# Performance work log

Hardware: AMD Instinct MI355X
Metric: run time of the kernel (lower is better)

The kernel has to match this reference:

```python
import jax, jax.numpy as jnp
import numpy as np

THRESH_FACTOR = 0.7


def ternarize(w):
    # w: [in_features, out_features]; per-row (dim 0) delta/alpha stats
    n = w.shape[1]
    abs_w = jnp.abs(w)
    delta = (THRESH_FACTOR / n) * abs_w.sum(axis=1, keepdims=True)  # [in, 1]
    mask = abs_w > delta
    count = mask.sum(axis=1, keepdims=True).astype(w.dtype)
    alpha = jnp.where(mask, abs_w, 0).sum(axis=1, keepdims=True) / count  # [in, 1]
    tern = jnp.where(w > delta, 1.0, jnp.where(w < -delta, -1.0, 0.0)).astype(w.dtype)
    return tern * alpha


def setup_inputs() -> dict:
    key = jax.random.key(0)
    k1, k2, k3 = jax.random.split(key, 3)
    B, IN, OUT = 8192, 4096, 4096
    x = jax.random.normal(k1, (B, IN), dtype=jnp.float32)
    # kaiming-uniform-ish then clamp to [-1, 1] as in the module
    bound_w = float(np.sqrt(6.0 / ((1.0 + 5.0) * IN)))
    weights = jax.random.uniform(k2, (IN, OUT), minval=-bound_w, maxval=bound_w, dtype=jnp.float32)
    weights = jnp.clip(weights, -1.0, 1.0)
    bound_b = 1.0 / float(np.sqrt(IN))
    bias = jax.random.uniform(k3, (OUT,), minval=-bound_b, maxval=bound_b, dtype=jnp.float32)
    return {"x": x, "weights": weights, "bias": bias}


def reference(x, weights, bias):
    w_t = ternarize(weights)
    return jnp.matmul(x, w_t) + bias
```

## Files before the change

### kernel.cpp

```cpp
#include <hip/hip_runtime.h>
#include <stdint.h>
#include <stddef.h>

#define IN_F 4096
#define OUT_F 4096

typedef int i32x4 __attribute__((ext_vector_type(4)));


__device__ static inline void async16(const void* g, void* l) {
    __builtin_amdgcn_global_load_lds(
        (const __attribute__((address_space(1))) unsigned int*)g,
        (__attribute__((address_space(3))) unsigned int*)l,
        16, 0, 0);
}

__device__ static inline double wred_d(double v) {
#pragma unroll
    for (int o = 32; o > 0; o >>= 1) v += __shfl_down(v, o, 64);
    return v;
}

__device__ static inline int wred_i(int v) {
#pragma unroll
    for (int o = 32; o > 0; o >>= 1) v += __shfl_down(v, o, 64);
    return v;
}

__device__ static inline float wred_max(float v) {
#pragma unroll
    for (int o = 32; o > 0; o >>= 1) v = fmaxf(v, __shfl_down(v, o, 64));
    return v;
}


__global__ __launch_bounds__(256) void rowstats_tern_kernel(
    const float* __restrict__ w,
    float* __restrict__ alpha_o,
    unsigned int* __restrict__ Tp) {
    __shared__ double sh_s[4], sh_m[4];
    __shared__ int sh_c[4];
    const int row = blockIdx.x;
    const int t = threadIdx.x;
    const int lane = t & 63, wv = t >> 6;
    const float4* wr = (const float4*)(w + (size_t)row * OUT_F);

    float4 v[4];
    double s = 0.0;
#pragma unroll
    for (int it = 0; it < 4; ++it) {
        v[it] = wr[t + it * 256];
        s += (double)fabsf(v[it].x) + (double)fabsf(v[it].y) +
             (double)fabsf(v[it].z) + (double)fabsf(v[it].w);
    }
    double sw = wred_d(s);
    if (lane == 0) sh_s[wv] = sw;
    __syncthreads();
    const double delta = (sh_s[0] + sh_s[1] + sh_s[2] + sh_s[3]) *
                         (0.7 / (double)OUT_F);

    unsigned int* trow = Tp + (size_t)row * (OUT_F / 4);
    double ms = 0.0;
    int cnt = 0;
#pragma unroll
    for (int it = 0; it < 4; ++it) {
        float f[4] = {v[it].x, v[it].y, v[it].z, v[it].w};
        unsigned int u = 0;
#pragma unroll
        for (int j = 0; j < 4; ++j) {
            double a = (double)fabsf(f[j]);
            if (a > delta) { ms += a; ++cnt; }
            int q = ((double)f[j] > delta) ? 1 :
                    (((double)f[j] < -delta) ? -1 : 0);
            u |= (unsigned int)(q & 0xff) << (j * 8);
        }
        trow[t + it * 256] = u;
    }
    double msw = wred_d(ms);
    int cw = wred_i(cnt);
    if (lane == 0) { sh_m[wv] = msw; sh_c[wv] = cw; }
    __syncthreads();
    if (t == 0) {
        double mtot = sh_m[0] + sh_m[1] + sh_m[2] + sh_m[3];
        int ctot = sh_c[0] + sh_c[1] + sh_c[2] + sh_c[3];
        alpha_o[row] = (float)(mtot / (double)ctot);
    }
}


__global__ __launch_bounds__(256) void transpose_i8_kernel(
    const unsigned int* __restrict__ Tp,
    int8_t* __restrict__ Tt) {
    __shared__ unsigned int ldsb[128 * 33];
    const int t = threadIdx.x;
    const int i0 = blockIdx.y * 128;
    const int j0 = blockIdx.x * 128;

#pragma unroll
    for (int it = 0; it < 4; ++it) {
        int bb = it * 256 + t;
        int rg = bb >> 5;
        int cc = bb & 31;
        unsigned int col[4] = {0u, 0u, 0u, 0u};
#pragma unroll
        for (int k = 0; k < 4; ++k) {
            unsigned int d = Tp[(size_t)(i0 + rg * 4 + k) * (OUT_F / 4) +
                                (j0 >> 2) + cc];
            col[0] |= (d & 0xffu) << (k * 8);
            col[1] |= ((d >> 8) & 0xffu) << (k * 8);
            col[2] |= ((d >> 16) & 0xffu) << (k * 8);
            col[3] |= ((d >> 24) & 0xffu) << (k * 8);
        }
#pragma unroll
        for (int j = 0; j < 4; ++j)
            ldsb[(cc * 4 + j) * 33 + rg] = col[j];
    }
    __syncthreads();
#pragma unroll
    for (int it = 0; it < 4; ++it) {
        int idx = it * 256 + t;
        int rr = idx >> 3;
        int c2 = idx & 7;
        uint4 o;
        o.x = ldsb[rr * 33 + c2 * 4 + 0];
        o.y = ldsb[rr * 33 + c2 * 4 + 1];
        o.z = ldsb[rr * 33 + c2 * 4 + 2];
        o.w = ldsb[rr * 33 + c2 * 4 + 3];
        *(uint4*)(Tt + (size_t)(j0 + rr) * IN_F + i0 + c2 * 16) = o;
    }
}


__global__ __launch_bounds__(256) void xquant_kernel(
    const float* __restrict__ x,
    const float* __restrict__ alpha,
    int8_t* __restrict__ xq,
    float* __restrict__ scale_o) {
    __shared__ float sh_mx[4];
    const int row = blockIdx.x;
    const int t = threadIdx.x;
    const int lane = t & 63, wv = t >> 6;
    const float4* xr = (const float4*)(x + (size_t)row * IN_F);
    const float4* ar = (const float4*)alpha;

    float4 xs[4];
    float mx = 0.0f;
#pragma unroll
    for (int it = 0; it < 4; ++it) {
        float4 v = xr[t + it * 256];
        float4 a = ar[t + it * 256];
        v.x *= a.x; v.y *= a.y; v.z *= a.z; v.w *= a.w;
        xs[it] = v;
        mx = fmaxf(mx, fmaxf(fmaxf(fabsf(v.x), fabsf(v.y)),
                             fmaxf(fabsf(v.z), fabsf(v.w))));
    }
    float mw = wred_max(mx);
    if (lane == 0) sh_mx[wv] = mw;
    __syncthreads();
    const float rmax = fmaxf(fmaxf(sh_mx[0], sh_mx[1]), fmaxf(sh_mx[2], sh_mx[3]));
    const float inv = (rmax > 0.0f) ? (127.0f / rmax) : 0.0f;

    unsigned int* qd = (unsigned int*)(xq + (size_t)row * IN_F);
#pragma unroll
    for (int it = 0; it < 4; ++it) {
        float f[4] = {xs[it].x, xs[it].y, xs[it].z, xs[it].w};
        unsigned int u = 0;
#pragma unroll
        for (int j = 0; j < 4; ++j) {
            int q = __float2int_rn(f[j] * inv);
            u |= (unsigned int)(q & 0xff) << (j * 8);
        }
        qd[t + it * 256] = u;
    }
    if (t == 0) scale_o[row] = (rmax > 0.0f) ? (rmax / 127.0f) : 1.0f;
}


#define GBARRIER() asm volatile("s_barrier" ::: "memory")

#define STAGE(G, GR0, TILE, LBASE, HALF)                                        \
    do {                                                                        \
        _Pragma("unroll")                                                       \
        for (int rr_ = 0; rr_ < 2; ++rr_) {                                     \
            const int L_ = (HALF) * 1024 + rr_ * 512 + t;                       \
            const int row_ = L_ >> 3;                                           \
            const int gch_ = (L_ & 7) ^ (row_ & 7);                             \
            async16((G) + (size_t)((GR0) + row_) * IN_F + (TILE) * 128 +        \
                        (gch_ << 4),                                            \
                    (LBASE) + (L_ << 4));                                       \
        }                                                                       \
    } while (0)

#define READ_A(BUF, MI0)                                                        \
    _Pragma("unroll")                                                           \
    for (int mi_ = 0; mi_ < 4; ++mi_) {                                         \
        a[2 * mi_]     = *(const i32x4*)((BUF) + offA_k0 + ((MI0) + mi_) * 2048); \
        a[2 * mi_ + 1] = *(const i32x4*)((BUF) + offA_k1 + ((MI0) + mi_) * 2048); \
    }

#define READ_B(BUF, NI0, DST)                                                   \
    _Pragma("unroll")                                                           \
    for (int ni_ = 0; ni_ < 2; ++ni_) {                                         \
        DST[2 * ni_]     = *(const i32x4*)((BUF) + offB_k0 + ((NI0) + ni_) * 2048); \
        DST[2 * ni_ + 1] = *(const i32x4*)((BUF) + offB_k1 + ((NI0) + ni_) * 2048); \
    }

#define MFMA_Q(MI0, NI0, BSRC)                                                  \
    do {                                                                        \
        __builtin_amdgcn_s_setprio(1);                                          \
        _Pragma("unroll")                                                       \
        for (int mi_ = 0; mi_ < 4; ++mi_) {                                     \
            _Pragma("unroll")                                                   \
            for (int ni_ = 0; ni_ < 2; ++ni_) {                                 \
                acc[(MI0) + mi_][(NI0) + ni_] =                                 \
                    __builtin_amdgcn_mfma_i32_16x16x64_i8(                      \
                        a[2 * mi_], BSRC[2 * ni_],                              \
                        acc[(MI0) + mi_][(NI0) + ni_], 0, 0, 0);                \
                acc[(MI0) + mi_][(NI0) + ni_] =                                 \
                    __builtin_amdgcn_mfma_i32_16x16x64_i8(                      \
                        a[2 * mi_ + 1], BSRC[2 * ni_ + 1],                      \
                        acc[(MI0) + mi_][(NI0) + ni_], 0, 0, 0);                \
            }                                                                   \
        }                                                                       \
        __builtin_amdgcn_s_setprio(0);                                          \
    } while (0)

__global__ __launch_bounds__(512, 2) void gemm_i8_8ph(
    const int8_t* __restrict__ Xq,
    const int8_t* __restrict__ Tq,
    const float* __restrict__ scale,
    const float* __restrict__ bias,
    float* __restrict__ out) {
    extern __shared__ __align__(16) int8_t lds[];
    const int K = IN_F;
    const int NT = K / 128;
    const int NI = NT / 2;

    const int t = threadIdx.x;
    const int lane = t & 63;
    const int wave = t >> 6;
    const int lm = lane & 15;
    const int qh = lane >> 4;
    const int wm = (wave >> 2) << 7;
    const int wn = (wave & 3) << 6;

    const int nwg = gridDim.x;
    const int id = blockIdx.x;
    const int swz = (id & 7) * (nwg >> 3) + (id >> 3);
    const int m0 = (swz >> 4) << 8;
    const int n0 = (swz & 15) << 8;

    int8_t* const A0  = lds;
    int8_t* const B0  = lds + 32768;
    int8_t* const A1b = lds + 65536;
    int8_t* const B1b = lds + 98304;

    const int swzs = lm & 7;
    const int offA_k0 = (wm + lm) * 128 + ((qh ^ swzs) << 4);
    const int offA_k1 = (wm + lm) * 128 + (((4 + qh) ^ swzs) << 4);
    const int offB_k0 = (wn + lm) * 128 + ((qh ^ swzs) << 4);
    const int offB_k1 = (wn + lm) * 128 + (((4 + qh) ^ swzs) << 4);

    i32x4 acc[8][4];
#pragma unroll
    for (int i = 0; i < 8; ++i)
#pragma unroll
        for (int j = 0; j < 4; ++j)
#pragma unroll
            for (int r = 0; r < 4; ++r) acc[i][j][r] = 0;

    i32x4 a[8], bA[4], bB[4];

    STAGE(Xq, m0, 0, A0, 0);
    STAGE(Xq, m0, 0, A0, 1);
    STAGE(Tq, n0, 0, B0, 0);
    STAGE(Tq, n0, 0, B0, 1);
    STAGE(Tq, n0, 1, B1b, 0);
    STAGE(Tq, n0, 1, B1b, 1);
    asm volatile("s_waitcnt vmcnt(4)" ::: "memory");
    GBARRIER();

#pragma unroll 1
    for (int i = 0; i < NI; ++i) {
        const int kt = 2 * i;
        READ_A(A0, 0);
        READ_B(B0, 0, bA);
        READ_B(B0, 2, bB);
        STAGE(Xq, m0, kt + 1, A1b, 0);
        STAGE(Xq, m0, kt + 1, A1b, 1);
        GBARRIER();
        MFMA_Q(0, 0, bA);
        MFMA_Q(0, 2, bB);
        GBARRIER();
        READ_A(A0, 4);
        if (kt + 2 < NT) {
            STAGE(Tq, n0, kt + 2, B0, 0);
            STAGE(Tq, n0, kt + 2, B0, 1);
        }
        GBARRIER();
        MFMA_Q(4, 0, bA);
        MFMA_Q(4, 2, bB);
        asm volatile("s_waitcnt vmcnt(4)" ::: "memory");
        GBARRIER();
        READ_A(A1b, 0);
        READ_B(B1b, 0, bA);
        READ_B(B1b, 2, bB);
        if (kt + 2 < NT) {
            STAGE(Xq, m0, kt + 2, A0, 0);
            STAGE(Xq, m0, kt + 2, A0, 1);
        }
        GBARRIER();
        MFMA_Q(0, 0, bA);
        MFMA_Q(0, 2, bB);
        GBARRIER();
        READ_A(A1b, 4);
        if (kt + 3 < NT) {
            STAGE(Tq, n0, kt + 3, B1b, 0);
            STAGE(Tq, n0, kt + 3, B1b, 1);
        }
        GBARRIER();
        MFMA_Q(4, 0, bA);
        MFMA_Q(4, 2, bB);
        if (i + 1 < NI) asm volatile("s_waitcnt vmcnt(4)" ::: "memory");
        else            asm volatile("s_waitcnt vmcnt(0)" ::: "memory");
        GBARRIER();
    }

    const int q4 = qh << 2;
#pragma unroll
    for (int mi = 0; mi < 8; ++mi) {
        float sc[4];
#pragma unroll
        for (int r = 0; r < 4; ++r) sc[r] = scale[m0 + wm + mi * 16 + q4 + r];
#pragma unroll
        for (int ni = 0; ni < 4; ++ni) {
            int col = n0 + wn + ni * 16 + lm;
            float b = bias[col];
#pragma unroll
            for (int r = 0; r < 4; ++r) {
                int row = m0 + wm + mi * 16 + q4 + r;
                out[(size_t)row * OUT_F + col] =
                    (float)acc[mi][ni][r] * sc[r] + b;
            }
        }
    }
}


extern "C" void kernel_launch(void* const* d_in, const int* in_sizes, int n_in,
                              void* d_out, int out_size, void* d_ws, size_t ws_size,
                              hipStream_t stream) {
    const float* x = (const float*)d_in[0];
    const float* w = (const float*)d_in[1];
    const float* bias = (const float*)d_in[2];
    float* out = (float*)d_out;
    const int B = in_sizes[0] / IN_F;

    char* ws = (char*)d_ws;
    int8_t* Tt = (int8_t*)ws;
    unsigned int* Tp = (unsigned int*)(ws + (size_t)16777216);
    int8_t* Xq = (int8_t*)(ws + (size_t)16777216);
    float* alpha = (float*)(ws + (size_t)50331648);
    float* scale = (float*)(ws + (size_t)50331648 + 16384);

    static int lds_set = 0;
    if (!lds_set) {
        hipFuncSetAttribute((const void*)gemm_i8_8ph,
                            hipFuncAttributeMaxDynamicSharedMemorySize, 131072);
        lds_set = 1;
    }

    rowstats_tern_kernel<<<IN_F, 256, 0, stream>>>(w, alpha, Tp);
    transpose_i8_kernel<<<dim3(OUT_F / 128, IN_F / 128), 256, 0, stream>>>(Tp, Tt);
    xquant_kernel<<<B, 256, 0, stream>>>(x, alpha, Xq, scale);
    const int nwg = (B / 256) * (OUT_F / 256);
    gemm_i8_8ph<<<dim3(nwg), dim3(512), 131072, stream>>>(Xq, Tt, scale, bias, out);
}
```

Before: 385.2 us.

## Fuse ternarize-transpose with x quantization and trim GEMM barriers

Row stats now store only alpha and delta in device globals. One merged kernel then either quantizes rows of x or re-reads w, ternarizes it against the stored delta and writes it transposed. This drops the packed Tp intermediate and one launch, and the two independent jobs run in the same grid. In the GEMM main loop, four s_barriers between LDS reads plus staging and the MFMAs are removed, and the waitcnt is made conditional, to reduce sync stalls. This risks LDS read/write races if the staging targets overlap buffers still being read.

```diff
diff --git a/kernel.cpp b/kernel.cpp
--- a/kernel.cpp
+++ b/kernel.cpp
@@ -6,6 +6,10 @@
 #define OUT_F 4096
 
 typedef int i32x4 __attribute__((ext_vector_type(4)));
+
+__device__ float  g_alpha[IN_F];
+__device__ double g_delta[IN_F];
+__device__ float  g_scale[8192];
 
 
 __device__ static inline void async16(const void* g, void* l) {
@@ -34,10 +38,8 @@
 }
 
 
-__global__ __launch_bounds__(256) void rowstats_tern_kernel(
-    const float* __restrict__ w,
-    float* __restrict__ alpha_o,
-    unsigned int* __restrict__ Tp) {
+__global__ __launch_bounds__(256) void rowstats_kernel(
+    const float* __restrict__ w) {
     __shared__ double sh_s[4], sh_m[4];
     __shared__ int sh_c[4];
     const int row = blockIdx.x;
@@ -59,22 +61,16 @@
     const double delta = (sh_s[0] + sh_s[1] + sh_s[2] + sh_s[3]) *
                          (0.7 / (double)OUT_F);
 
-    unsigned int* trow = Tp + (size_t)row * (OUT_F / 4);
     double ms = 0.0;
     int cnt = 0;
 #pragma unroll
     for (int it = 0; it < 4; ++it) {
         float f[4] = {v[it].x, v[it].y, v[it].z, v[it].w};
-        unsigned int u = 0;
 #pragma unroll
         for (int j = 0; j < 4; ++j) {
             double a = (double)fabsf(f[j]);
             if (a > delta) { ms += a; ++cnt; }
-            int q = ((double)f[j] > delta) ? 1 :
-                    (((double)f[j] < -delta) ? -1 : 0);
-            u |= (unsigned int)(q & 0xff) << (j * 8);
-        }
-        trow[t + it * 256] = u;
+        }
     }
     double msw = wred_d(ms);
     int cw = wred_i(cnt);
@@ -83,96 +79,99 @@
     if (t == 0) {
         double mtot = sh_m[0] + sh_m[1] + sh_m[2] + sh_m[3];
         int ctot = sh_c[0] + sh_c[1] + sh_c[2] + sh_c[3];
-        alpha_o[row] = (float)(mtot / (double)ctot);
-    }
-}
-
-
-__global__ __launch_bounds__(256) void transpose_i8_kernel(
-    const unsigned int* __restrict__ Tp,
-    int8_t* __restrict__ Tt) {
-    __shared__ unsigned int ldsb[128 * 33];
+        g_alpha[row] = (float)(mtot / (double)ctot);
+        g_delta[row] = delta;
+    }
+}
+
+
+__global__ __launch_bounds__(256) void fused_tq(
+    const float* __restrict__ w,
+    const float* __restrict__ x,
+    int8_t* __restrict__ Xq,
+    int8_t* __restrict__ Tt,
+    int nxq) {
+    __shared__ __align__(16) unsigned int ldsb[128 * 33];
     const int t = threadIdx.x;
-    const int i0 = blockIdx.y * 128;
-    const int j0 = blockIdx.x * 128;
-
-#pragma unroll
-    for (int it = 0; it < 4; ++it) {
-        int bb = it * 256 + t;
-        int rg = bb >> 5;
-        int cc = bb & 31;
-        unsigned int col[4] = {0u, 0u, 0u, 0u};
-#pragma unroll
-        for (int k = 0; k < 4; ++k) {
-            unsigned int d = Tp[(size_t)(i0 + rg * 4 + k) * (OUT_F / 4) +
-                                (j0 >> 2) + cc];
-            col[0] |= (d & 0xffu) << (k * 8);
-            col[1] |= ((d >> 8) & 0xffu) << (k * 8);
-            col[2] |= ((d >> 16) & 0xffu) << (k * 8);
-            col[3] |= ((d >> 24) & 0xffu) << (k * 8);
-        }
-#pragma unroll
-        for (int j = 0; j < 4; ++j)
-            ldsb[(cc * 4 + j) * 33 + rg] = col[j];
-    }
-    __syncthreads();
-#pragma unroll
-    for (int it = 0; it < 4; ++it) {
-        int idx = it * 256 + t;
-        int rr = idx >> 3;
-        int c2 = idx & 7;
-        uint4 o;
-        o.x = ldsb[rr * 33 + c2 * 4 + 0];
-        o.y = ldsb[rr * 33 + c2 * 4 + 1];
-        o.z = ldsb[rr * 33 + c2 * 4 + 2];
-        o.w = ldsb[rr * 33 + c2 * 4 + 3];
-        *(uint4*)(Tt + (size_t)(j0 + rr) * IN_F + i0 + c2 * 16) = o;
-    }
-}
-
-
-__global__ __launch_bounds__(256) void xquant_kernel(
-    const float* __restrict__ x,
-    const float* __restrict__ alpha,
-    int8_t* __restrict__ xq,
-    float* __restrict__ scale_o) {
-    __shared__ float sh_mx[4];
-    const int row = blockIdx.x;
-    const int t = threadIdx.x;
-    const int lane = t & 63, wv = t >> 6;
-    const float4* xr = (const float4*)(x + (size_t)row * IN_F);
-    const float4* ar = (const float4*)alpha;
-
-    float4 xs[4];
-    float mx = 0.0f;
-#pragma unroll
-    for (int it = 0; it < 4; ++it) {
-        float4 v = xr[t + it * 256];
-        float4 a = ar[t + it * 256];
-        v.x *= a.x; v.y *= a.y; v.z *= a.z; v.w *= a.w;
-        xs[it] = v;
-        mx = fmaxf(mx, fmaxf(fmaxf(fabsf(v.x), fabsf(v.y)),
-                             fmaxf(fabsf(v.z), fabsf(v.w))));
-    }
-    float mw = wred_max(mx);
-    if (lane == 0) sh_mx[wv] = mw;
-    __syncthreads();
-    const float rmax = fmaxf(fmaxf(sh_mx[0], sh_mx[1]), fmaxf(sh_mx[2], sh_mx[3]));
-    const float inv = (rmax > 0.0f) ? (127.0f / rmax) : 0.0f;
-
-    unsigned int* qd = (unsigned int*)(xq + (size_t)row * IN_F);
-#pragma unroll
-    for (int it = 0; it < 4; ++it) {
-        float f[4] = {xs[it].x, xs[it].y, xs[it].z, xs[it].w};
-        unsigned int u = 0;
-#pragma unroll
-        for (int j = 0; j < 4; ++j) {
-            int q = __float2int_rn(f[j] * inv);
-            u |= (unsigned int)(q & 0xff) << (j * 8);
-        }
-        qd[t + it * 256] = u;
-    }
-    if (t == 0) scale_o[row] = (rmax > 0.0f) ? (rmax / 127.0f) : 1.0f;
+
+    if ((int)blockIdx.x < nxq) {
+        float* sh_mx = (float*)ldsb;
+        const int row = blockIdx.x;
+        const int lane = t & 63, wv = t >> 6;
+        const float4* xr = (const float4*)(x + (size_t)row * IN_F);
+        const float4* ar = (const float4*)g_alpha;
+
+        float4 xs[4];
+        float mx = 0.0f;
+#pragma unroll
+        for (int it = 0; it < 4; ++it) {
+            float4 v = xr[t + it * 256];
+            float4 a = ar[t + it * 256];
+            v.x *= a.x; v.y *= a.y; v.z *= a.z; v.w *= a.w;
+            xs[it] = v;
+            mx = fmaxf(mx, fmaxf(fmaxf(fabsf(v.x), fabsf(v.y)),
+                                 fmaxf(fabsf(v.z), fabsf(v.w))));
+        }
+        float mw = wred_max(mx);
+        if (lane == 0) sh_mx[wv] = mw;
+        __syncthreads();
+        const float rmax = fmaxf(fmaxf(sh_mx[0], sh_mx[1]),
+                                 fmaxf(sh_mx[2], sh_mx[3]));
+        const float inv = (rmax > 0.0f) ? (127.0f / rmax) : 0.0f;
+
+        unsigned int* qd = (unsigned int*)(Xq + (size_t)row * IN_F);
+#pragma unroll
+        for (int it = 0; it < 4; ++it) {
+            float f[4] = {xs[it].x, xs[it].y, xs[it].z, xs[it].w};
+            unsigned int u = 0;
+#pragma unroll
+            for (int j = 0; j < 4; ++j) {
+                int q = __float2int_rn(f[j] * inv);
+                u |= (unsigned int)(q & 0xff) << (j * 8);
+            }
+            qd[t + it * 256] = u;
+        }
+        if (t == 0) g_scale[row] = (rmax > 0.0f) ? (rmax / 127.0f) : 1.0f;
+    } else {
+        const int tt = blockIdx.x - nxq;
+        const int i0 = (tt >> 5) * 128;
+        const int j0 = (tt & 31) * 128;
+#pragma unroll
+        for (int it = 0; it < 4; ++it) {
+            int bb = it * 256 + t;
+            int rg = bb >> 5;
+            int cc = bb & 31;
+            unsigned int col[4] = {0u, 0u, 0u, 0u};
+#pragma unroll
+            for (int k = 0; k < 4; ++k) {
+                int irow = i0 + rg * 4 + k;
+                float4 v = *(const float4*)(w + (size_t)irow * OUT_F + j0 + cc * 4);
+                double d = g_delta[irow];
+                float f[4] = {v.x, v.y, v.z, v.w};
+#pragma unroll
+                for (int j = 0; j < 4; ++j) {
+                    int q = ((double)f[j] > d) ? 1 : (((double)f[j] < -d) ? -1 : 0);
+                    col[j] |= (unsigned int)(q & 0xff) << (k * 8);
+                }
+            }
+#pragma unroll
+            for (int j = 0; j < 4; ++j)
+                ldsb[(cc * 4 + j) * 33 + rg] = col[j];
+        }
+        __syncthreads();
+#pragma unroll
+        for (int it = 0; it < 4; ++it) {
+            int idx = it * 256 + t;
+            int rr = idx >> 3;
+            int c2 = idx & 7;
+            uint4 o;
+            o.x = ldsb[rr * 33 + c2 * 4 + 0];
+            o.y = ldsb[rr * 33 + c2 * 4 + 1];
+            o.z = ldsb[rr * 33 + c2 * 4 + 2];
+            o.w = ldsb[rr * 33 + c2 * 4 + 3];
+            *(uint4*)(Tt + (size_t)(j0 + rr) * IN_F + i0 + c2 * 16) = o;
+        }
+    }
 }
 
 
@@ -228,7 +227,6 @@
 __global__ __launch_bounds__(512, 2) void gemm_i8_8ph(
     const int8_t* __restrict__ Xq,
     const int8_t* __restrict__ Tq,
-    const float* __restrict__ scale,
     const float* __restrict__ bias,
     float* __restrict__ out) {
     extern __shared__ __align__(16) int8_t lds[];
@@ -288,7 +286,6 @@
         READ_B(B0, 2, bB);
         STAGE(Xq, m0, kt + 1, A1b, 0);
         STAGE(Xq, m0, kt + 1, A1b, 1);
-        GBARRIER();
         MFMA_Q(0, 0, bA);
         MFMA_Q(0, 2, bB);
         GBARRIER();
@@ -297,10 +294,10 @@
             STAGE(Tq, n0, kt + 2, B0, 0);
             STAGE(Tq, n0, kt + 2, B0, 1);
         }
-        GBARRIER();
         MFMA_Q(4, 0, bA);
         MFMA_Q(4, 2, bB);
-        asm volatile("s_waitcnt vmcnt(4)" ::: "memory");
+        if (i + 1 < NI) asm volatile("s_waitcnt vmcnt(4)" ::: "memory");
+        else            asm volatile("s_waitcnt vmcnt(0)" ::: "memory");
         GBARRIER();
         READ_A(A1b, 0);
         READ_B(B1b, 0, bA);
@@ -309,7 +306,6 @@
             STAGE(Xq, m0, kt + 2, A0, 0);
             STAGE(Xq, m0, kt + 2, A0, 1);
         }
-        GBARRIER();
         MFMA_Q(0, 0, bA);
         MFMA_Q(0, 2, bB);
         GBARRIER();
@@ -318,7 +314,6 @@
             STAGE(Tq, n0, kt + 3, B1b, 0);
             STAGE(Tq, n0, kt + 3, B1b, 1);
         }
-        GBARRIER();
         MFMA_Q(4, 0, bA);
         MFMA_Q(4, 2, bB);
         if (i + 1 < NI) asm volatile("s_waitcnt vmcnt(4)" ::: "memory");
@@ -331,7 +326,7 @@
     for (int mi = 0; mi < 8; ++mi) {
         float sc[4];
 #pragma unroll
-        for (int r = 0; r < 4; ++r) sc[r] = scale[m0 + wm + mi * 16 + q4 + r];
+        for (int r = 0; r < 4; ++r) sc[r] = g_scale[m0 + wm + mi * 16 + q4 + r];
 #pragma unroll
         for (int ni = 0; ni < 4; ++ni) {
             int col = n0 + wn + ni * 16 + lm;
@@ -358,10 +353,7 @@
 
     char* ws = (char*)d_ws;
     int8_t* Tt = (int8_t*)ws;
-    unsigned int* Tp = (unsigned int*)(ws + (size_t)16777216);
     int8_t* Xq = (int8_t*)(ws + (size_t)16777216);
-    float* alpha = (float*)(ws + (size_t)50331648);
-    float* scale = (float*)(ws + (size_t)50331648 + 16384);
 
     static int lds_set = 0;
     if (!lds_set) {
@@ -370,9 +362,8 @@
         lds_set = 1;
     }
 
-    rowstats_tern_kernel<<<IN_F, 256, 0, stream>>>(w, alpha, Tp);
-    transpose_i8_kernel<<<dim3(OUT_F / 128, IN_F / 128), 256, 0, stream>>>(Tp, Tt);
-    xquant_kernel<<<B, 256, 0, stream>>>(x, alpha, Xq, scale);
+    rowstats_kernel<<<IN_F, 256, 0, stream>>>(w);
+    fused_tq<<<B + (IN_F / 128) * (OUT_F / 128), 256, 0, stream>>>(w, x, Xq, Tt, B);
     const int nwg = (B / 256) * (OUT_F / 256);
-    gemm_i8_8ph<<<dim3(nwg), dim3(512), 131072, stream>>>(Xq, Tt, scale, bias, out);
-}
+    gemm_i8_8ph<<<dim3(nwg), dim3(512), 131072, stream>>>(Xq, Tt, bias, out);
+}
```

After: 377.0 us. 2.1% less time.
